# Kernel optimization log

Measured on AMD Instinct MI355X. Metric: run time of the kernel, lower is better.

The kernel has to match this reference:

```python
import jax, jax.numpy as jnp
import numpy as np

RES = (64, 128, 256)          # res_plane per scale
CDIM = (32, 32, 32)           # plane_feat_dim per scale
PADDING = 0.1
EPS = 1e-5                    # torch code uses 10e-6
PLANE_AXES = {"xz": (0, 2), "xy": (0, 1), "yz": (1, 2)}


def _plane_features(coord, feats, plane, res):
    """coord: (B,N,3) float, feats: (B,N,C) float -> (B,C,res,res).
    Faithful to normalize_coordinate + coordinate2index + scatter_mean."""
    a, b = PLANE_AXES[plane]
    xy = jnp.stack([coord[..., a], coord[..., b]], axis=-1)   # (B,N,2)
    xy = xy / (1.0 + PADDING + EPS) + 0.5
    xy = jnp.clip(xy, 0.0, 1.0 - EPS)
    ij = (xy * res).astype(jnp.int32)                         # trunc == floor (nonneg)
    idx = ij[..., 0] + res * ij[..., 1]                       # (B,N) flattened grid index
    r2 = res * res

    def per_batch(f, i):  # f: (N,C), i: (N,)
        s = jax.ops.segment_sum(f, i, num_segments=r2)        # (R2,C) scatter-add
        c = jax.ops.segment_sum(jnp.ones((f.shape[0],), f.dtype), i, num_segments=r2)
        return s / jnp.maximum(c, 1.0)[:, None]               # scatter_mean: div by clamp(count,1)

    out = jax.vmap(per_batch)(feats, idx)                     # (B,R2,C)
    B, _, C = out.shape
    return out.transpose(0, 2, 1).reshape(B, C, res, res)


def _forward(f_list, c_list):
    # returns tuple over 3 scales, each a tuple (xz, xy, yz) of (B,C,res,res)
    return tuple(
        tuple(_plane_features(c, f, pl, r) for pl in ("xz", "xy", "yz"))
        for f, c, r in zip(f_list, c_list, RES)
    )


def setup_inputs() -> dict:
    key = jax.random.key(0)
    ks = jax.random.split(key, 6)
    B = 8
    Ns = (65536, 32768, 16384)
    inp = {}
    for i, (n, c) in enumerate(zip(Ns, CDIM)):
        inp[f"f{i}"] = jax.random.normal(ks[i], (B, n, c), dtype=jnp.float32)
        # coords in [-0.5, 0.5): normalize maps them into [0,1) grid range
        inp[f"c{i}"] = jax.random.uniform(ks[3 + i], (B, n, 3), dtype=jnp.float32) - 0.5
    return inp


def reference(f0, f1, f2, c0, c1, c2):
    return _forward((f0, f1, f2), (c0, c1, c2))
```

## Files before the change

kernel.cpp:

```cpp
#include <hip/hip_runtime.h>

static constexpr int B = 8;
static constexpr int C = 32;

static constexpr size_t CNT0 = 0,        CNT1 = 98304,    CNT2 = 491520;
static constexpr size_t CNT_TOTAL = 2064384;
static constexpr size_t OFF0 = 2064384,  OFF1 = 2162688,  OFF2 = 2555904;
static constexpr size_t REC0 = 4128768,  REC1 = 5701632,  REC2 = 6488064;
static constexpr size_t LIST0 = 13762560, LIST1 = 15335424, LIST2 = 16121856;
static constexpr size_t OUT0 = 0, OUT1 = 3145728, OUT2 = 15728640;

__device__ __forceinline__ void plane_cells(float x, float y, float z, int res,
                                            int idxs[3])
{
#pragma clang fp contract(off)
    constexpr float denomf = (float)(1.0 + 0.1 + 1e-5);
    constexpr float recipf = 1.0f / denomf;
    constexpr float hi     = (float)(1.0 - 1e-5);
    const float rf = (float)res;
    const float tx = x * recipf;
    const float ty = y * recipf;
    const float tz = z * recipf;
    const float ux = fminf(fmaxf(tx + 0.5f, 0.0f), hi);
    const float uy = fminf(fmaxf(ty + 0.5f, 0.0f), hi);
    const float uz = fminf(fmaxf(tz + 0.5f, 0.0f), hi);
    const int ix = (int)(ux * rf);
    const int iy = (int)(uy * rf);
    const int iz = (int)(uz * rf);
    idxs[0] = ix + res * iz;
    idxs[1] = ix + res * iy;
    idxs[2] = iy + res * iz;
}

__global__ __launch_bounds__(256) void fused_count_rank(
    const float* __restrict__ c0, const float* __restrict__ c1,
    const float* __restrict__ c2, unsigned int* __restrict__ ws)
{
    int blk = blockIdx.x;
    const float* coords; int N, res, shift; size_t cntB, recB;
    if (blk < 2048)      { coords = c0; N = 65536; res = 64;  shift = 8; cntB = CNT0; recB = REC0; }
    else if (blk < 3072) { blk -= 2048; coords = c1; N = 32768; res = 128; shift = 7; cntB = CNT1; recB = REC1; }
    else                 { blk -= 3072; coords = c2; N = 16384; res = 256; shift = 6; cntB = CNT2; recB = REC2; }
    const int b = blk >> shift;
    const int p = ((blk & ((1 << shift) - 1)) << 8) + threadIdx.x;
    const size_t pt = (size_t)b * N + p;
    const float x = coords[pt * 3 + 0];
    const float y = coords[pt * 3 + 1];
    const float z = coords[pt * 3 + 2];
    int idxs[3];
    plane_cells(x, y, z, res, idxs);
    const int R2 = res * res;
    unsigned int* cnt = ws + cntB;
    unsigned int* rec = ws + recB;
#pragma unroll
    for (int k = 0; k < 3; ++k) {
        const unsigned int cell = (unsigned int)idxs[k];
        const unsigned int rank =
            atomicAdd(&cnt[((size_t)k * B + b) * R2 + cell], 1u);
        rec[((size_t)k * B + b) * N + p] = (cell << 16) | rank;
    }
}

__global__ __launch_bounds__(1024) void fused_scan(unsigned int* __restrict__ ws)
{
    __shared__ unsigned int sdata[1024];
    int blk = blockIdx.x;
    size_t cntB, offB; int R2;
    if (blk < 24)      {              cntB = CNT0; offB = OFF0; R2 = 4096; }
    else if (blk < 48) { blk -= 24;   cntB = CNT1; offB = OFF1; R2 = 16384; }
    else               { blk -= 48;   cntB = CNT2; offB = OFF2; R2 = 65536; }
    const size_t base = (size_t)blk * (size_t)R2;
    const uint4* cnt4 = (const uint4*)(ws + cntB + base);
    uint4* off4 = (uint4*)(ws + offB + base);
    const int E4 = R2 >> 12;
    const int tid = threadIdx.x;
    unsigned int tsum = 0;
    for (int i = 0; i < E4; ++i) {
        const uint4 cc = cnt4[tid * E4 + i];
        tsum += cc.x + cc.y + cc.z + cc.w;
    }
    sdata[tid] = tsum;
    __syncthreads();
    for (int d = 1; d < 1024; d <<= 1) {
        unsigned int v = (tid >= d) ? sdata[tid - d] : 0u;
        __syncthreads();
        sdata[tid] += v;
        __syncthreads();
    }
    unsigned int run = sdata[tid] - tsum;
    for (int i = 0; i < E4; ++i) {
        const uint4 cc = cnt4[tid * E4 + i];
        uint4 o;
        o.x = run; run += cc.x;
        o.y = run; run += cc.y;
        o.z = run; run += cc.z;
        o.w = run; run += cc.w;
        off4[tid * E4 + i] = o;
    }
}

__global__ __launch_bounds__(256) void fused_build_list(unsigned int* __restrict__ ws)
{
    int blk = blockIdx.x;
    int N, R2, shift; size_t recB, offB, listB;
    if (blk < 6144)      {              N = 65536; R2 = 4096;  shift = 8; recB = REC0; offB = OFF0; listB = LIST0; }
    else if (blk < 9216) { blk -= 6144; N = 32768; R2 = 16384; shift = 7; recB = REC1; offB = OFF1; listB = LIST1; }
    else                 { blk -= 9216; N = 16384; R2 = 65536; shift = 6; recB = REC2; offB = OFF2; listB = LIST2; }
    const int kb = blk >> shift;
    const int p = ((blk & ((1 << shift) - 1)) << 8) + threadIdx.x;
    const unsigned int* rec = ws + recB;
    const unsigned int* off = ws + offB;
    unsigned short* list = (unsigned short*)ws + listB;
    const unsigned int r = rec[(size_t)kb * N + p];
    const unsigned int cell = r >> 16;
    const unsigned int rank = r & 0xffffu;
    const unsigned int pos = off[(size_t)kb * R2 + cell] + rank;
    list[(size_t)kb * N + pos] = (unsigned short)p;
}

__global__ __launch_bounds__(256) void fused_gather_mean(
    const float* __restrict__ f0, const float* __restrict__ f1,
    const float* __restrict__ f2, const unsigned int* __restrict__ ws,
    float* __restrict__ out)
{
    __shared__ float tile[C][64 + 1];
    __shared__ unsigned int s_cnt[64];
    __shared__ unsigned int s_off[64];
    int blk = blockIdx.x;
    const float* feats; int N, R2, shift; size_t cntB, offB, listB, outB;
    if (blk < 1536)      {              feats = f0; N = 65536; R2 = 4096;  shift = 6;  cntB = CNT0; offB = OFF0; listB = LIST0; outB = OUT0; }
    else if (blk < 7680) { blk -= 1536; feats = f1; N = 32768; R2 = 16384; shift = 8;  cntB = CNT1; offB = OFF1; listB = LIST1; outB = OUT1; }
    else                 { blk -= 7680; feats = f2; N = 16384; R2 = 65536; shift = 10; cntB = CNT2; offB = OFF2; listB = LIST2; outB = OUT2; }
    const int kb = blk >> shift;
    const int cellBase = (blk & ((1 << shift) - 1)) << 6;
    const int b = kb & (B - 1);
    const int h   = threadIdx.x >> 5;
    const int sub = (threadIdx.x >> 3) & 3;
    const int chq = threadIdx.x & 7;
    const size_t segBase  = (size_t)kb * R2;
    const size_t listBase = (size_t)kb * N;
    const unsigned short* list = (const unsigned short*)ws + listB;
    const char* fB = (const char*)(feats + (size_t)b * N * C);
    const unsigned int laneOff = (unsigned int)chq << 4;

    if (threadIdx.x < 64) {
        s_cnt[threadIdx.x] = ws[cntB + segBase + cellBase + threadIdx.x];
        s_off[threadIdx.x] = ws[offB + segBase + cellBase + threadIdx.x];
    }
    __syncthreads();

    for (int i = 0; i < 8; ++i) {
        const int lc = h * 8 + i;
        const unsigned int n = s_cnt[lc];
        if (n == 0u) {
            if (sub == 0) {
                tile[chq * 4 + 0][lc] = 0.0f;
                tile[chq * 4 + 1][lc] = 0.0f;
                tile[chq * 4 + 2][lc] = 0.0f;
                tile[chq * 4 + 3][lc] = 0.0f;
            }
            continue;
        }
        const unsigned short* lp = list + listBase + s_off[lc];
        float ax = 0.0f, ay = 0.0f, az = 0.0f, aw = 0.0f;
        unsigned int j = 0;
        for (; j + 8 <= n; j += 8) {
            const unsigned int oA = ((unsigned int)lp[j + sub]     << 7) + laneOff;
            const unsigned int oB = ((unsigned int)lp[j + 4 + sub] << 7) + laneOff;
            const float4 vA = *(const float4*)(fB + oA);
            const float4 vB = *(const float4*)(fB + oB);
            ax += vA.x + vB.x; ay += vA.y + vB.y;
            az += vA.z + vB.z; aw += vA.w + vB.w;
        }
        if (j + sub < n) {
            const unsigned int o = ((unsigned int)lp[j + sub] << 7) + laneOff;
            const float4 v = *(const float4*)(fB + o);
            ax += v.x; ay += v.y; az += v.z; aw += v.w;
        }
        if (j + 4 + sub < n) {
            const unsigned int o = ((unsigned int)lp[j + 4 + sub] << 7) + laneOff;
            const float4 v = *(const float4*)(fB + o);
            ax += v.x; ay += v.y; az += v.z; aw += v.w;
        }
        ax += __shfl_xor(ax, 8);  ay += __shfl_xor(ay, 8);
        az += __shfl_xor(az, 8);  aw += __shfl_xor(aw, 8);
        ax += __shfl_xor(ax, 16); ay += __shfl_xor(ay, 16);
        az += __shfl_xor(az, 16); aw += __shfl_xor(aw, 16);
        if (sub == 0) {
            const float r = __builtin_amdgcn_rcpf((float)n);
            tile[chq * 4 + 0][lc] = ax * r;
            tile[chq * 4 + 1][lc] = ay * r;
            tile[chq * 4 + 2][lc] = az * r;
            tile[chq * 4 + 3][lc] = aw * r;
        }
    }
    __syncthreads();
#pragma unroll
    for (int c8 = 0; c8 < 8; ++c8) {
        const int ch2  = c8 * 4 + (threadIdx.x >> 6);
        const int cell = threadIdx.x & 63;
        __builtin_nontemporal_store(
            tile[ch2][cell],
            &out[outB + ((size_t)kb * C + ch2) * R2 + cellBase + cell]);
    }
}

extern "C" void kernel_launch(void* const* d_in, const int* in_sizes, int n_in,
                              void* d_out, int out_size, void* d_ws, size_t ws_size,
                              hipStream_t stream)
{
    const float *f[3], *c[3];
    const bool interleaved = in_sizes[1] < in_sizes[2];
    if (interleaved) {
        f[0] = (const float*)d_in[0]; c[0] = (const float*)d_in[1];
        f[1] = (const float*)d_in[2]; c[1] = (const float*)d_in[3];
        f[2] = (const float*)d_in[4]; c[2] = (const float*)d_in[5];
    } else {
        f[0] = (const float*)d_in[0]; f[1] = (const float*)d_in[1];
        f[2] = (const float*)d_in[2];
        c[0] = (const float*)d_in[3]; c[1] = (const float*)d_in[4];
        c[2] = (const float*)d_in[5];
    }

    unsigned int* ws32 = (unsigned int*)d_ws;
    float* out = (float*)d_out;

    hipMemsetAsync(d_ws, 0, CNT_TOTAL * sizeof(unsigned int), stream);

    fused_count_rank<<<dim3(3584), 256, 0, stream>>>(c[0], c[1], c[2], ws32);
    fused_scan<<<dim3(72), 1024, 0, stream>>>(ws32);
    fused_build_list<<<dim3(10752), 256, 0, stream>>>(ws32);
    fused_gather_mean<<<dim3(32256), 256, 0, stream>>>(f[0], f[1], f[2], ws32, out);
}
```

Before: 616.2 us.

## Interleave batch/plane block ordering and vectorize gather output stores

New measurement: 619.1 us. About the same (+0.5%).

```diff
diff --git a/kernel.cpp b/kernel.cpp
--- a/kernel.cpp
+++ b/kernel.cpp
@@ -2,6 +2,8 @@
 
 static constexpr int B = 8;
 static constexpr int C = 32;
+
+typedef float vfloat4 __attribute__((ext_vector_type(4)));
 
 static constexpr size_t CNT0 = 0,        CNT1 = 98304,    CNT2 = 491520;
 static constexpr size_t CNT_TOTAL = 2064384;
@@ -37,12 +39,12 @@
     const float* __restrict__ c2, unsigned int* __restrict__ ws)
 {
     int blk = blockIdx.x;
-    const float* coords; int N, res, shift; size_t cntB, recB;
-    if (blk < 2048)      { coords = c0; N = 65536; res = 64;  shift = 8; cntB = CNT0; recB = REC0; }
-    else if (blk < 3072) { blk -= 2048; coords = c1; N = 32768; res = 128; shift = 7; cntB = CNT1; recB = REC1; }
-    else                 { blk -= 3072; coords = c2; N = 16384; res = 256; shift = 6; cntB = CNT2; recB = REC2; }
-    const int b = blk >> shift;
-    const int p = ((blk & ((1 << shift) - 1)) << 8) + threadIdx.x;
+    const float* coords; int N, res; size_t cntB, recB;
+    if (blk < 2048)      {              coords = c0; N = 65536; res = 64;  cntB = CNT0; recB = REC0; }
+    else if (blk < 3072) { blk -= 2048; coords = c1; N = 32768; res = 128; cntB = CNT1; recB = REC1; }
+    else                 { blk -= 3072; coords = c2; N = 16384; res = 256; cntB = CNT2; recB = REC2; }
+    const int b = blk & 7;
+    const int p = (blk >> 3) * 256 + threadIdx.x;
     const size_t pt = (size_t)b * N + p;
     const float x = coords[pt * 3 + 0];
     const float y = coords[pt * 3 + 1];
@@ -102,12 +104,13 @@
 __global__ __launch_bounds__(256) void fused_build_list(unsigned int* __restrict__ ws)
 {
     int blk = blockIdx.x;
-    int N, R2, shift; size_t recB, offB, listB;
-    if (blk < 6144)      {              N = 65536; R2 = 4096;  shift = 8; recB = REC0; offB = OFF0; listB = LIST0; }
-    else if (blk < 9216) { blk -= 6144; N = 32768; R2 = 16384; shift = 7; recB = REC1; offB = OFF1; listB = LIST1; }
-    else                 { blk -= 9216; N = 16384; R2 = 65536; shift = 6; recB = REC2; offB = OFF2; listB = LIST2; }
-    const int kb = blk >> shift;
-    const int p = ((blk & ((1 << shift) - 1)) << 8) + threadIdx.x;
+    int N, R2; size_t recB, offB, listB;
+    if (blk < 6144)      {              N = 65536; R2 = 4096;  recB = REC0; offB = OFF0; listB = LIST0; }
+    else if (blk < 9216) { blk -= 6144; N = 32768; R2 = 16384; recB = REC1; offB = OFF1; listB = LIST1; }
+    else                 { blk -= 9216; N = 16384; R2 = 65536; recB = REC2; offB = OFF2; listB = LIST2; }
+    const int kb    = blk % 24;
+    const int chunk = blk / 24;
+    const int p = chunk * 256 + threadIdx.x;
     const unsigned int* rec = ws + recB;
     const unsigned int* off = ws + offB;
     unsigned short* list = (unsigned short*)ws + listB;
@@ -123,16 +126,16 @@
     const float* __restrict__ f2, const unsigned int* __restrict__ ws,
     float* __restrict__ out)
 {
-    __shared__ float tile[C][64 + 1];
+    __shared__ float tile[C][68];
     __shared__ unsigned int s_cnt[64];
     __shared__ unsigned int s_off[64];
     int blk = blockIdx.x;
-    const float* feats; int N, R2, shift; size_t cntB, offB, listB, outB;
-    if (blk < 1536)      {              feats = f0; N = 65536; R2 = 4096;  shift = 6;  cntB = CNT0; offB = OFF0; listB = LIST0; outB = OUT0; }
-    else if (blk < 7680) { blk -= 1536; feats = f1; N = 32768; R2 = 16384; shift = 8;  cntB = CNT1; offB = OFF1; listB = LIST1; outB = OUT1; }
-    else                 { blk -= 7680; feats = f2; N = 16384; R2 = 65536; shift = 10; cntB = CNT2; offB = OFF2; listB = LIST2; outB = OUT2; }
-    const int kb = blk >> shift;
-    const int cellBase = (blk & ((1 << shift) - 1)) << 6;
+    const float* feats; int N, R2; size_t cntB, offB, listB, outB;
+    if (blk < 1536)      {              feats = f0; N = 65536; R2 = 4096;  cntB = CNT0; offB = OFF0; listB = LIST0; outB = OUT0; }
+    else if (blk < 7680) { blk -= 1536; feats = f1; N = 32768; R2 = 16384; cntB = CNT1; offB = OFF1; listB = LIST1; outB = OUT1; }
+    else                 { blk -= 7680; feats = f2; N = 16384; R2 = 65536; cntB = CNT2; offB = OFF2; listB = LIST2; outB = OUT2; }
+    const int kb       = blk % 24;
+    const int cellBase = (blk / 24) * 64;
     const int b = kb & (B - 1);
     const int h   = threadIdx.x >> 5;
     const int sub = (threadIdx.x >> 3) & 3;
@@ -195,13 +198,16 @@
         }
     }
     __syncthreads();
+    {
+        const int ch2 = threadIdx.x >> 3;
+        const int g   = threadIdx.x & 7;
+        float* orow = out + outB + ((size_t)kb * C + ch2) * R2 + cellBase;
 #pragma unroll
-    for (int c8 = 0; c8 < 8; ++c8) {
-        const int ch2  = c8 * 4 + (threadIdx.x >> 6);
-        const int cell = threadIdx.x & 63;
-        __builtin_nontemporal_store(
-            tile[ch2][cell],
-            &out[outB + ((size_t)kb * C + ch2) * R2 + cellBase + cell]);
+        for (int gg = 0; gg < 2; ++gg) {
+            const int grp = g + gg * 8;
+            const vfloat4 v = *(const vfloat4*)&tile[ch2][grp * 4];
+            __builtin_nontemporal_store(v, (vfloat4*)(orow + grp * 4));
+        }
     }
 }
 
```
